# Performance work log

Measured on AMD Instinct MI355X. Metric: run time of the kernel, lower is better.

The kernel has to match this reference:

```python
import jax, jax.numpy as jnp
import numpy as np

N_NODES, N_EDGES, N_ANGLES, D = 20000, 200000, 600000, 128
BN_EPS = 1e-5
AGG_EPS = 1e-6


def _bn(x, gamma, beta):
    # training-mode BatchNorm1d over the node/edge batch dim
    mu = jnp.mean(x, axis=0)
    var = jnp.var(x, axis=0)
    return gamma * (x - mu) * jax.lax.rsqrt(var + BN_EPS) + beta


def _gcao(x, edge_index, y, W, b, bn):
    # Edge-gated graph conv (GCAO). W:[5,d,d] rows = src_gate, dst_gate,
    # edge_gate, src_update, dst_update. bn:[4,d] = gamma_n, beta_n, gamma_e, beta_e.
    src, dst = edge_index[0], edge_index[1]
    lin = lambda i, v: v @ W[i] + b[i]
    m = lin(0, x)[src] + lin(1, x)[dst] + lin(2, y)          # [E, d] edge messages
    sigma = jax.nn.sigmoid(m)                                 # edge gates
    bh = lin(3, x)[src] * sigma                               # gated src messages
    n = x.shape[0]
    num = jax.ops.segment_sum(bh, dst, num_segments=n)        # [N, d]
    den = jax.ops.segment_sum(sigma, dst, num_segments=n) + AGG_EPS
    x_new = x + jax.nn.silu(_bn(lin(4, x) + num / den, bn[0], bn[1]))
    y_new = y + jax.nn.silu(_bn(m, bn[2], bn[3]))
    return x_new, y_new


def setup_inputs() -> dict:
    key = jax.random.key(0)
    ks = jax.random.split(key, 8)
    s = 1.0 / np.sqrt(D)
    bn_init = jnp.stack([jnp.ones(D), jnp.zeros(D), jnp.ones(D), jnp.zeros(D)]).astype(jnp.float32)
    return {
        "atom_feats": jax.random.normal(ks[0], (N_NODES, D), jnp.float32),
        "bond_attr": jax.random.normal(ks[1], (N_EDGES, D), jnp.float32),
        "triplet_feats": jax.random.normal(ks[2], (N_ANGLES, D), jnp.float32),
        "edge_index": jax.random.randint(ks[3], (2, N_EDGES), 0, N_NODES),
        "angle_index": jax.random.randint(ks[4], (2, N_ANGLES), 0, N_EDGES),
        "W_ba": jax.random.normal(ks[5], (5, D, D), jnp.float32) * s,
        "b_ba": jnp.zeros((5, D), jnp.float32),
        "bn_ba": bn_init,
        "W_ab": jax.random.normal(ks[6], (5, D, D), jnp.float32) * s,
        "b_ab": jnp.zeros((5, D), jnp.float32),
        "bn_ab": bn_init,
    }


def reference(atom_feats, bond_attr, triplet_feats, edge_index, angle_index,
              W_ba, b_ba, bn_ba, W_ab, b_ab, bn_ab):
    # bondAndAngleUpdate: line graph (nodes=bonds, edges=angles)
    bond, trip = _gcao(bond_attr, angle_index, triplet_feats, W_ba, b_ba, bn_ba)
    # bondAndAtomUpdate: atom graph (nodes=atoms, edges=bonds)
    atom, bond_new = _gcao(atom_feats, edge_index, bond, W_ab, b_ab, bn_ab)
    return atom, bond_new, trip
```

## Files before the change

kernel.cpp:

```cpp
#include <hip/hip_runtime.h>
#include <hip/hip_bf16.h>


typedef float f32x4 __attribute__((ext_vector_type(4)));
typedef short s16x8 __attribute__((ext_vector_type(8)));
typedef unsigned short u16;

__device__ __forceinline__ u16 f2bf(float f){
  union { float f; unsigned u; } v; v.f = f;
  unsigned u = v.u;
  return (u16)((u + 0x7FFFu + ((u >> 16) & 1u)) >> 16);
}
__device__ __forceinline__ float bf2f(u16 h){
  union { unsigned u; float f; } v; v.u = ((unsigned)h) << 16; return v.f;
}
__device__ __forceinline__ float sigmoidf_(float x){ return 1.0f / (1.0f + __expf(-x)); }
__device__ __forceinline__ float siluf_(float x){ return x / (1.0f + __expf(-x)); }

__global__ __launch_bounds__(256) void pack_w_kernel(
    const float* __restrict__ Wba, const float* __restrict__ Wab, u16* __restrict__ wpack){
  int idx = blockIdx.x * 256 + threadIdx.x;
  int mat = idx >> 14;
  int r = idx & 16383;
  int j = r & 7, lane = (r >> 3) & 63, ks = (r >> 9) & 3, t = r >> 11;
  int k = ks * 32 + ((lane >> 4) << 3) + j;
  int n = t * 16 + (lane & 15);
  const float* W = (mat < 5) ? (Wba + (size_t)mat * 16384) : (Wab + (size_t)(mat - 5) * 16384);
  wpack[idx] = f2bf(W[k * 128 + n]);
}

__global__ __launch_bounds__(256) void xmm_kernel(
    const float* __restrict__ x, int nrows,
    const u16* __restrict__ wpackL, const float* __restrict__ bias,
    u16* __restrict__ L03, u16* __restrict__ L1, u16* __restrict__ L4){
  __shared__ u16 wlds[16384];
  const int tid = threadIdx.x;
  const int lane = tid & 63, wv = tid >> 6;
  const int g = lane >> 4;
  const long row = (long)blockIdx.x * 64 + wv * 16 + (lane & 15);
  const bool valid = row < nrows;
  const long rc = valid ? row : (long)(nrows - 1);

  s16x8 xf[4];
  {
    const float* xr = x + rc * 128 + g * 8;
    #pragma unroll
    for (int ks = 0; ks < 4; ++ks){
      float4 a = *(const float4*)(xr + ks * 32);
      float4 b = *(const float4*)(xr + ks * 32 + 4);
      s16x8 f;
      f[0]=(short)f2bf(a.x); f[1]=(short)f2bf(a.y); f[2]=(short)f2bf(a.z); f[3]=(short)f2bf(a.w);
      f[4]=(short)f2bf(b.x); f[5]=(short)f2bf(b.y); f[6]=(short)f2bf(b.z); f[7]=(short)f2bf(b.w);
      xf[ks] = f;
    }
  }
  const int mats[4] = {0, 1, 3, 4};
  #pragma unroll
  for (int mi = 0; mi < 4; ++mi){
    const int mat = mats[mi];
    __syncthreads();
    { const uint4* s = (const uint4*)(wpackL + (size_t)mat * 16384);
      uint4* d = (uint4*)wlds;
      #pragma unroll
      for (int i = 0; i < 8; ++i) d[i * 256 + tid] = s[i * 256 + tid];
    }
    __syncthreads();
    #pragma unroll
    for (int t = 0; t < 8; ++t){
      f32x4 acc = {0.f, 0.f, 0.f, 0.f};
      #pragma unroll
      for (int ks = 0; ks < 4; ++ks){
        s16x8 wf = *(const s16x8*)(wlds + (t * 4 + ks) * 512 + lane * 8);
        acc = __builtin_amdgcn_mfma_f32_16x16x32_bf16(wf, xf[ks], acc, 0, 0, 0);
      }
      const int c0 = t * 16 + g * 4;
      float4 bv = *(const float4*)(bias + mat * 128 + c0);
      if (valid){
        ushort4 o;
        o.x = f2bf(acc[0] + bv.x); o.y = f2bf(acc[1] + bv.y);
        o.z = f2bf(acc[2] + bv.z); o.w = f2bf(acc[3] + bv.w);
        u16* dp;
        if (mi == 0)      dp = L03 + row * 256 + c0;
        else if (mi == 1) dp = L1  + row * 128 + c0;
        else if (mi == 2) dp = L03 + row * 256 + 128 + c0;
        else              dp = L4  + row * 128 + c0;
        *(ushort4*)dp = o;
      }
    }
  }
}

__global__ __launch_bounds__(256) void edge_gemm_kernel(
    const float* __restrict__ y, const int* __restrict__ pos,
    const u16* __restrict__ wpack2, const float* __restrict__ bias2,
    u16* __restrict__ BH){
  __shared__ u16 wlds[16384];
  const int tid = threadIdx.x;
  { const uint4* s = (const uint4*)wpack2;
    uint4* d = (uint4*)wlds;
    #pragma unroll
    for (int i = 0; i < 8; ++i) d[i * 256 + tid] = s[i * 256 + tid];
  }
  const int lane = tid & 63, wv = tid >> 6;
  const int g = lane >> 4;
  const int e = blockIdx.x * 64 + wv * 16 + (lane & 15);
  const int p = pos[e];
  s16x8 yf[4];
  {
    const float* yr = y + (size_t)e * 128 + g * 8;
    #pragma unroll
    for (int ks = 0; ks < 4; ++ks){
      float4 a = *(const float4*)(yr + ks * 32);
      float4 b = *(const float4*)(yr + ks * 32 + 4);
      s16x8 f;
      f[0]=(short)f2bf(a.x); f[1]=(short)f2bf(a.y); f[2]=(short)f2bf(a.z); f[3]=(short)f2bf(a.w);
      f[4]=(short)f2bf(b.x); f[5]=(short)f2bf(b.y); f[6]=(short)f2bf(b.z); f[7]=(short)f2bf(b.w);
      yf[ks] = f;
    }
  }
  __syncthreads();
  u16* mrow = BH + (size_t)p * 128;
  #pragma unroll
  for (int t = 0; t < 8; ++t){
    f32x4 acc = {0.f, 0.f, 0.f, 0.f};
    #pragma unroll
    for (int ks = 0; ks < 4; ++ks){
      s16x8 wf = *(const s16x8*)(wlds + (t * 4 + ks) * 512 + lane * 8);
      acc = __builtin_amdgcn_mfma_f32_16x16x32_bf16(wf, yf[ks], acc, 0, 0, 0);
    }
    const int c0 = t * 16 + g * 4;
    float4 bv = *(const float4*)(bias2 + c0);
    ushort4 o;
    o.x = f2bf(acc[0] + bv.x); o.y = f2bf(acc[1] + bv.y);
    o.z = f2bf(acc[2] + bv.z); o.w = f2bf(acc[3] + bv.w);
    *(ushort4*)(mrow + c0) = o;
  }
}

__global__ __launch_bounds__(256) void combine_kernel(
    const int* __restrict__ src_csr, const int* __restrict__ dst_csr,
    const u16* __restrict__ L03, const u16* __restrict__ L1,
    u16* __restrict__ M, u16* __restrict__ BH){
  const int tid = threadIdx.x;
  const int wv = tid >> 6, half = (tid >> 5) & 1, ln = tid & 31;
  const int p = blockIdx.x * 8 + wv * 2 + half;
  const int c = ln * 4;
  const int src = src_csr[p];
  const int dst = dst_csr[p];
  ushort4 ma = *(const ushort4*)(BH + (size_t)p * 128 + c);
  ushort4 l0 = *(const ushort4*)(L03 + (size_t)src * 256 + c);
  ushort4 l3 = *(const ushort4*)(L03 + (size_t)src * 256 + 128 + c);
  ushort4 l1 = *(const ushort4*)(L1 + (size_t)dst * 128 + c);
  float m0 = bf2f(ma.x) + bf2f(l0.x) + bf2f(l1.x);
  float m1 = bf2f(ma.y) + bf2f(l0.y) + bf2f(l1.y);
  float m2 = bf2f(ma.z) + bf2f(l0.z) + bf2f(l1.z);
  float m3 = bf2f(ma.w) + bf2f(l0.w) + bf2f(l1.w);
  float g0 = sigmoidf_(m0), g1 = sigmoidf_(m1), g2 = sigmoidf_(m2), g3 = sigmoidf_(m3);
  ushort4 mo; mo.x = f2bf(m0); mo.y = f2bf(m1); mo.z = f2bf(m2); mo.w = f2bf(m3);
  ushort4 bo;
  bo.x = f2bf(bf2f(l3.x) * g0); bo.y = f2bf(bf2f(l3.y) * g1);
  bo.z = f2bf(bf2f(l3.z) * g2); bo.w = f2bf(bf2f(l3.w) * g3);
  *(ushort4*)(M + (size_t)p * 128 + c) = mo;
  *(ushort4*)(BH + (size_t)p * 128 + c) = bo;
}

__global__ __launch_bounds__(256) void hist_kernel(
    const int* __restrict__ dstIdx, int ne, int* __restrict__ count){
  int e = blockIdx.x * 256 + threadIdx.x;
  if (e < ne) atomicAdd(&count[dstIdx[e]], 1);
}

__global__ __launch_bounds__(256) void scan1_kernel(
    const int* __restrict__ count, int n, int* __restrict__ offset, int* __restrict__ bsum){
  __shared__ int sh[256];
  const int tid = threadIdx.x;
  const int i0 = blockIdx.x * 1024 + tid * 4;
  int c0 = (i0 + 0 < n) ? count[i0 + 0] : 0;
  int c1 = (i0 + 1 < n) ? count[i0 + 1] : 0;
  int c2 = (i0 + 2 < n) ? count[i0 + 2] : 0;
  int c3 = (i0 + 3 < n) ? count[i0 + 3] : 0;
  int tsum = c0 + c1 + c2 + c3;
  sh[tid] = tsum;
  __syncthreads();
  int val = tsum;
  for (int d = 1; d < 256; d <<= 1){
    int t = (tid >= d) ? sh[tid - d] : 0;
    __syncthreads();
    val += t;
    sh[tid] = val;
    __syncthreads();
  }
  int run = val - tsum;
  if (i0 + 0 < n) offset[i0 + 0] = run; run += c0;
  if (i0 + 1 < n) offset[i0 + 1] = run; run += c1;
  if (i0 + 2 < n) offset[i0 + 2] = run; run += c2;
  if (i0 + 3 < n) offset[i0 + 3] = run;
  if (tid == 255) bsum[blockIdx.x] = val;
}

__global__ __launch_bounds__(256) void scan2_kernel(int* __restrict__ bsum, int nb){
  __shared__ int sh[256];
  const int tid = threadIdx.x;
  int v = (tid < nb) ? bsum[tid] : 0;
  sh[tid] = v;
  __syncthreads();
  int val = v;
  for (int d = 1; d < 256; d <<= 1){
    int t = (tid >= d) ? sh[tid - d] : 0;
    __syncthreads();
    val += t;
    sh[tid] = val;
    __syncthreads();
  }
  if (tid < nb) bsum[tid] = val - v;
}

__global__ __launch_bounds__(256) void scan3_kernel(
    int* __restrict__ offset, int n, const int* __restrict__ bsum, int* __restrict__ cursor){
  int i = blockIdx.x * 256 + threadIdx.x;
  if (i < n){
    int v = offset[i] + bsum[i >> 10];
    offset[i] = v;
    cursor[i] = v;
  }
}

__global__ __launch_bounds__(256) void scatter_kernel(
    const int* __restrict__ dstIdx, const int* __restrict__ srcIdx, int ne,
    int* __restrict__ cursor, int* __restrict__ pos,
    int* __restrict__ src_csr, int* __restrict__ dst_csr){
  int e = blockIdx.x * 256 + threadIdx.x;
  if (e < ne){
    int d = dstIdx[e];
    int p = atomicAdd(&cursor[d], 1);
    pos[e] = p;
    src_csr[p] = srcIdx[e];
    dst_csr[p] = d;
  }
}

__global__ __launch_bounds__(256) void agg2_kernel(
    const int* __restrict__ offset, const int* __restrict__ count,
    const u16* __restrict__ M, const u16* __restrict__ BH,
    const u16* __restrict__ L4, int n, u16* __restrict__ hbuf){
  const int node = blockIdx.x * 4 + (threadIdx.x >> 6);
  if (node >= n) return;
  const int c2 = (threadIdx.x & 63) * 2;
  const int start = offset[node], deg = count[node];
  float n0 = 0, n1 = 0, d0 = 0, d1 = 0;
  int i = 0;
  for (; i + 2 <= deg; i += 2){
    const u16* mr = M + (size_t)(start + i) * 128;
    const u16* br = BH + (size_t)(start + i) * 128;
    ushort2 m0 = *(const ushort2*)(mr + c2);
    ushort2 m1 = *(const ushort2*)(mr + 128 + c2);
    ushort2 b0 = *(const ushort2*)(br + c2);
    ushort2 b1 = *(const ushort2*)(br + 128 + c2);
    float g00 = sigmoidf_(bf2f(m0.x)), g01 = sigmoidf_(bf2f(m0.y));
    float g10 = sigmoidf_(bf2f(m1.x)), g11 = sigmoidf_(bf2f(m1.y));
    d0 += g00 + g10; d1 += g01 + g11;
    n0 += bf2f(b0.x) + bf2f(b1.x); n1 += bf2f(b0.y) + bf2f(b1.y);
  }
  if (i < deg){
    const u16* mr = M + (size_t)(start + i) * 128;
    const u16* br = BH + (size_t)(start + i) * 128;
    ushort2 m0 = *(const ushort2*)(mr + c2);
    ushort2 b0 = *(const ushort2*)(br + c2);
    d0 += sigmoidf_(bf2f(m0.x)); d1 += sigmoidf_(bf2f(m0.y));
    n0 += bf2f(b0.x); n1 += bf2f(b0.y);
  }
  ushort2 l4 = *(const ushort2*)(L4 + (size_t)node * 128 + c2);
  float h0 = bf2f(l4.x) + n0 / (d0 + 1e-6f);
  float h1 = bf2f(l4.y) + n1 / (d1 + 1e-6f);
  ushort2 ho; ho.x = f2bf(h0); ho.y = f2bf(h1);
  *(ushort2*)(hbuf + (size_t)node * 128 + c2) = ho;
}

__global__ __launch_bounds__(256) void colstats_kernel(
    const u16* __restrict__ M, int rows, int rstride,
    float* __restrict__ sum, float* __restrict__ sumsq){
  const int tid = threadIdx.x;
  const int c2 = (tid & 63) * 2, rg = tid >> 6;
  float s0=0,ss0=0,s1=0,ss1=0;
  for (long r = blockIdx.x * 4 + rg; r < rows; r += (long)gridDim.x * 4){
    ushort2 v = *(const ushort2*)(M + r * rstride + c2);
    float a = bf2f(v.x), b = bf2f(v.y);
    s0 += a; ss0 += a*a; s1 += b; ss1 += b*b;
  }
  __shared__ float sh[1024];
  sh[tid] = s0; sh[256+tid] = ss0; sh[512+tid] = s1; sh[768+tid] = ss1;
  __syncthreads();
  if (rg == 0){
    int c = tid & 63;
    float S0=0,SS0=0,S1=0,SS1=0;
    #pragma unroll
    for (int q = 0; q < 4; ++q){ int t2 = q*64 + c; S0+=sh[t2]; SS0+=sh[256+t2]; S1+=sh[512+t2]; SS1+=sh[768+t2]; }
    atomicAdd(&sum[c2], S0);   atomicAdd(&sumsq[c2], SS0);
    atomicAdd(&sum[c2+1], S1); atomicAdd(&sumsq[c2+1], SS1);
  }
}

__global__ __launch_bounds__(256) void apply_bf16_kernel(
    const float* __restrict__ base, const u16* __restrict__ m, int n,
    const float* __restrict__ sum, const float* __restrict__ sumsq,
    const float* __restrict__ gamma, const float* __restrict__ beta,
    float* __restrict__ out){
  const int tid = threadIdx.x;
  const int c2 = (tid & 63) * 2, rg = tid >> 6;
  const float invn = 1.0f / (float)n;
  float m0 = sum[c2] * invn, m1 = sum[c2+1] * invn;
  float v0 = sumsq[c2] * invn - m0*m0, v1 = sumsq[c2+1] * invn - m1*m1;
  float sc0 = gamma[c2]   * rsqrtf(v0 + 1e-5f);
  float sc1 = gamma[c2+1] * rsqrtf(v1 + 1e-5f);
  float sh0 = beta[c2]   - m0 * sc0;
  float sh1 = beta[c2+1] - m1 * sc1;
  for (long r = blockIdx.x * 4 + rg; r < n; r += (long)gridDim.x * 4){
    const long bi = r * 128 + c2;
    ushort2 mv = *(const ushort2*)(m + bi);
    float2 xv = *(const float2*)(base + bi);
    float a = bf2f(mv.x) * sc0 + sh0, b = bf2f(mv.y) * sc1 + sh1;
    *(float2*)(out + bi) = make_float2(xv.x + siluf_(a), xv.y + siluf_(b));
  }
}

__global__ __launch_bounds__(256) void apply_perm_kernel(
    const float* __restrict__ base, const u16* __restrict__ M,
    const int* __restrict__ pos, int n,
    const float* __restrict__ sum, const float* __restrict__ sumsq,
    const float* __restrict__ gamma, const float* __restrict__ beta,
    float* __restrict__ out){
  const int tid = threadIdx.x;
  const int c2 = (tid & 63) * 2, rg = tid >> 6;
  const float invn = 1.0f / (float)n;
  float m0 = sum[c2] * invn, m1 = sum[c2+1] * invn;
  float v0 = sumsq[c2] * invn - m0*m0, v1 = sumsq[c2+1] * invn - m1*m1;
  float sc0 = gamma[c2]   * rsqrtf(v0 + 1e-5f);
  float sc1 = gamma[c2+1] * rsqrtf(v1 + 1e-5f);
  float sh0 = beta[c2]   - m0 * sc0;
  float sh1 = beta[c2+1] - m1 * sc1;
  for (long r = blockIdx.x * 4 + rg; r < n; r += (long)gridDim.x * 4){
    const int p = pos[r];
    ushort2 mv = *(const ushort2*)(M + (size_t)p * 128 + c2);
    float2 xv = *(const float2*)(base + r * 128 + c2);
    float a = bf2f(mv.x) * sc0 + sh0, b = bf2f(mv.y) * sc1 + sh1;
    *(float2*)(out + r * 128 + c2) = make_float2(xv.x + siluf_(a), xv.y + siluf_(b));
  }
}

extern "C" void kernel_launch(void* const* d_in, const int* in_sizes, int n_in,
                              void* d_out, int out_size, void* d_ws, size_t ws_size,
                              hipStream_t stream){
  const float* atom = (const float*)d_in[0];
  const float* bond = (const float*)d_in[1];
  const float* trip = (const float*)d_in[2];
  const int*   eidx = (const int*)d_in[3];
  const int*   aidx = (const int*)d_in[4];
  const float* Wba  = (const float*)d_in[5];
  const float* bba  = (const float*)d_in[6];
  const float* bnba = (const float*)d_in[7];
  const float* Wab  = (const float*)d_in[8];
  const float* bab  = (const float*)d_in[9];
  const float* bnab = (const float*)d_in[10];

  const int N = 20000, E = 200000, A = 600000;

  float* out_atom = (float*)d_out;
  float* out_bond = out_atom + (size_t)N * 128;
  float* out_trip = out_bond + (size_t)E * 128;

  char* ws = (char*)d_ws;
  u16* wpack = (u16*)ws;
  float* stats = (float*)(ws + 327680);
  float* sum_e = stats, *sumsq_e = stats + 128, *sum_n = stats + 256, *sumsq_n = stats + 384;
  int* bsum    = (int*)(ws + 329728);
  int* count   = (int*)(ws + 330752);
  int* offset  = (int*)(ws + 1130752);
  int* cursor  = (int*)(ws + 1930752);
  int* pos     = (int*)(ws + 2730752);
  int* src_csr = (int*)(ws + 5130752);
  int* dst_csr = (int*)(ws + 7530752);
  size_t off = 9930752;
  u16* L03 = (u16*)(ws + off); off += (size_t)E * 256 * 2;
  u16* L1  = (u16*)(ws + off); off += (size_t)E * 128 * 2;
  u16* L4  = (u16*)(ws + off); off += (size_t)E * 128 * 2;
  u16* M   = (u16*)(ws + off); off += (size_t)A * 128 * 2;
  u16* BH  = (u16*)(ws + off); off += (size_t)A * 128 * 2;
  u16* hbuf = L03;

  pack_w_kernel<<<640, 256, 0, stream>>>(Wba, Wab, wpack);

  {
    const int n = E, ne = A;
    const int* sIdx = aidx, *dIdx = aidx + A;
    hipMemsetAsync(stats, 0, 2048, stream);
    hipMemsetAsync(count, 0, (size_t)n * 4, stream);
    hist_kernel<<<(ne + 255) / 256, 256, 0, stream>>>(dIdx, ne, count);
    scan1_kernel<<<(n + 1023) / 1024, 256, 0, stream>>>(count, n, offset, bsum);
    scan2_kernel<<<1, 256, 0, stream>>>(bsum, (n + 1023) / 1024);
    scan3_kernel<<<(n + 255) / 256, 256, 0, stream>>>(offset, n, bsum, cursor);
    scatter_kernel<<<(ne + 255) / 256, 256, 0, stream>>>(dIdx, sIdx, ne, cursor, pos,
                                                         src_csr, dst_csr);
    xmm_kernel<<<n / 64, 256, 0, stream>>>(bond, n, wpack, bba, L03, L1, L4);
    edge_gemm_kernel<<<ne / 64, 256, 0, stream>>>(trip, pos, wpack + 2 * 16384,
                                                  bba + 256, BH);
    combine_kernel<<<ne / 8, 256, 0, stream>>>(src_csr, dst_csr, L03, L1, M, BH);
    colstats_kernel<<<1024, 256, 0, stream>>>(M, ne, 128, sum_e, sumsq_e);
    agg2_kernel<<<(n + 3) / 4, 256, 0, stream>>>(offset, count, M, BH, L4, n, hbuf);
    colstats_kernel<<<1024, 256, 0, stream>>>(hbuf, n, 128, sum_n, sumsq_n);
    apply_bf16_kernel<<<2048, 256, 0, stream>>>(bond, hbuf, n, sum_n, sumsq_n,
                                                bnba, bnba + 128, out_bond);
    apply_perm_kernel<<<2048, 256, 0, stream>>>(trip, M, pos, ne, sum_e, sumsq_e,
                                                bnba + 256, bnba + 384, out_trip);
  }

  {
    const int n = N, ne = E;
    const int* sIdx = eidx, *dIdx = eidx + E;
    hipMemsetAsync(stats, 0, 2048, stream);
    hipMemsetAsync(count, 0, (size_t)n * 4, stream);
    hist_kernel<<<(ne + 255) / 256, 256, 0, stream>>>(dIdx, ne, count);
    scan1_kernel<<<(n + 1023) / 1024, 256, 0, stream>>>(count, n, offset, bsum);
    scan2_kernel<<<1, 256, 0, stream>>>(bsum, (n + 1023) / 1024);
    scan3_kernel<<<(n + 255) / 256, 256, 0, stream>>>(offset, n, bsum, cursor);
    scatter_kernel<<<(ne + 255) / 256, 256, 0, stream>>>(dIdx, sIdx, ne, cursor, pos,
                                                         src_csr, dst_csr);
    xmm_kernel<<<(n + 63) / 64, 256, 0, stream>>>(atom, n, wpack + 5 * 16384, bab, L03, L1, L4);
    edge_gemm_kernel<<<ne / 64, 256, 0, stream>>>(out_bond, pos, wpack + 7 * 16384,
                                                  bab + 256, BH);
    combine_kernel<<<ne / 8, 256, 0, stream>>>(src_csr, dst_csr, L03, L1, M, BH);
    colstats_kernel<<<1024, 256, 0, stream>>>(M, ne, 128, sum_e, sumsq_e);
    agg2_kernel<<<(n + 3) / 4, 256, 0, stream>>>(offset, count, M, BH, L4, n, hbuf);
    colstats_kernel<<<1024, 256, 0, stream>>>(hbuf, n, 128, sum_n, sumsq_n);
    apply_bf16_kernel<<<2048, 256, 0, stream>>>(atom, hbuf, n, sum_n, sumsq_n,
                                                bnab, bnab + 128, out_atom);
    apply_perm_kernel<<<2048, 256, 0, stream>>>(out_bond, M, pos, ne, sum_e, sumsq_e,
                                                bnab + 256, bnab + 384, out_bond);
  }
}
```

Before: 1.227 ms.

## Fuse edge GEMM with gate combine, drop CSR src/dst arrays

Merges the edge-feature GEMM and the combine step into one kernel. The GEMM result is staged in LDS and combined with the gathered src/dst node projections in original edge order, and M and BH are written to their CSR positions. This removes a full bf16 round trip of the edge message through global memory and one launch, and lets scatter drop the src_csr/dst_csr writes. The two memsets are merged into one. In exchange, the extra LDS per block may lower occupancy.

```diff
diff --git a/kernel.cpp b/kernel.cpp
--- a/kernel.cpp
+++ b/kernel.cpp
@@ -90,11 +90,15 @@
   }
 }
 
-__global__ __launch_bounds__(256) void edge_gemm_kernel(
-    const float* __restrict__ y, const int* __restrict__ pos,
+__global__ __launch_bounds__(256) void edge_fused_kernel(
+    const float* __restrict__ y,
+    const int* __restrict__ srcIdx, const int* __restrict__ dstIdx,
+    const int* __restrict__ pos,
     const u16* __restrict__ wpack2, const float* __restrict__ bias2,
-    u16* __restrict__ BH){
+    const u16* __restrict__ L03, const u16* __restrict__ L1,
+    u16* __restrict__ M, u16* __restrict__ BH){
   __shared__ u16 wlds[16384];
+  __shared__ u16 mlds[64 * 132];
   const int tid = threadIdx.x;
   { const uint4* s = (const uint4*)wpack2;
     uint4* d = (uint4*)wlds;
@@ -103,8 +107,8 @@
   }
   const int lane = tid & 63, wv = tid >> 6;
   const int g = lane >> 4;
-  const int e = blockIdx.x * 64 + wv * 16 + (lane & 15);
-  const int p = pos[e];
+  const int erow = wv * 16 + (lane & 15);
+  const int e = blockIdx.x * 64 + erow;
   s16x8 yf[4];
   {
     const float* yr = y + (size_t)e * 128 + g * 8;
@@ -119,7 +123,6 @@
     }
   }
   __syncthreads();
-  u16* mrow = BH + (size_t)p * 128;
   #pragma unroll
   for (int t = 0; t < 8; ++t){
     f32x4 acc = {0.f, 0.f, 0.f, 0.f};
@@ -133,35 +136,34 @@
     ushort4 o;
     o.x = f2bf(acc[0] + bv.x); o.y = f2bf(acc[1] + bv.y);
     o.z = f2bf(acc[2] + bv.z); o.w = f2bf(acc[3] + bv.w);
-    *(ushort4*)(mrow + c0) = o;
-  }
-}
-
-__global__ __launch_bounds__(256) void combine_kernel(
-    const int* __restrict__ src_csr, const int* __restrict__ dst_csr,
-    const u16* __restrict__ L03, const u16* __restrict__ L1,
-    u16* __restrict__ M, u16* __restrict__ BH){
-  const int tid = threadIdx.x;
-  const int wv = tid >> 6, half = (tid >> 5) & 1, ln = tid & 31;
-  const int p = blockIdx.x * 8 + wv * 2 + half;
+    *(ushort4*)(mlds + erow * 132 + c0) = o;
+  }
+  __syncthreads();
+  const int hw = tid >> 5, ln = tid & 31;
   const int c = ln * 4;
-  const int src = src_csr[p];
-  const int dst = dst_csr[p];
-  ushort4 ma = *(const ushort4*)(BH + (size_t)p * 128 + c);
-  ushort4 l0 = *(const ushort4*)(L03 + (size_t)src * 256 + c);
-  ushort4 l3 = *(const ushort4*)(L03 + (size_t)src * 256 + 128 + c);
-  ushort4 l1 = *(const ushort4*)(L1 + (size_t)dst * 128 + c);
-  float m0 = bf2f(ma.x) + bf2f(l0.x) + bf2f(l1.x);
-  float m1 = bf2f(ma.y) + bf2f(l0.y) + bf2f(l1.y);
-  float m2 = bf2f(ma.z) + bf2f(l0.z) + bf2f(l1.z);
-  float m3 = bf2f(ma.w) + bf2f(l0.w) + bf2f(l1.w);
-  float g0 = sigmoidf_(m0), g1 = sigmoidf_(m1), g2 = sigmoidf_(m2), g3 = sigmoidf_(m3);
-  ushort4 mo; mo.x = f2bf(m0); mo.y = f2bf(m1); mo.z = f2bf(m2); mo.w = f2bf(m3);
-  ushort4 bo;
-  bo.x = f2bf(bf2f(l3.x) * g0); bo.y = f2bf(bf2f(l3.y) * g1);
-  bo.z = f2bf(bf2f(l3.z) * g2); bo.w = f2bf(bf2f(l3.w) * g3);
-  *(ushort4*)(M + (size_t)p * 128 + c) = mo;
-  *(ushort4*)(BH + (size_t)p * 128 + c) = bo;
+  #pragma unroll
+  for (int it = 0; it < 8; ++it){
+    const int es = it * 8 + hw;
+    const int ee = blockIdx.x * 64 + es;
+    const int p = pos[ee];
+    const int src = srcIdx[ee];
+    const int dst = dstIdx[ee];
+    ushort4 ma = *(const ushort4*)(mlds + es * 132 + c);
+    ushort4 l0 = *(const ushort4*)(L03 + (size_t)src * 256 + c);
+    ushort4 l3 = *(const ushort4*)(L03 + (size_t)src * 256 + 128 + c);
+    ushort4 l1 = *(const ushort4*)(L1 + (size_t)dst * 128 + c);
+    float m0 = bf2f(ma.x) + bf2f(l0.x) + bf2f(l1.x);
+    float m1 = bf2f(ma.y) + bf2f(l0.y) + bf2f(l1.y);
+    float m2 = bf2f(ma.z) + bf2f(l0.z) + bf2f(l1.z);
+    float m3 = bf2f(ma.w) + bf2f(l0.w) + bf2f(l1.w);
+    float g0 = sigmoidf_(m0), g1 = sigmoidf_(m1), g2 = sigmoidf_(m2), g3 = sigmoidf_(m3);
+    ushort4 mo; mo.x = f2bf(m0); mo.y = f2bf(m1); mo.z = f2bf(m2); mo.w = f2bf(m3);
+    ushort4 bo;
+    bo.x = f2bf(bf2f(l3.x) * g0); bo.y = f2bf(bf2f(l3.y) * g1);
+    bo.z = f2bf(bf2f(l3.z) * g2); bo.w = f2bf(bf2f(l3.w) * g3);
+    *(ushort4*)(M + (size_t)p * 128 + c) = mo;
+    *(ushort4*)(BH + (size_t)p * 128 + c) = bo;
+  }
 }
 
 __global__ __launch_bounds__(256) void hist_kernel(
@@ -226,16 +228,11 @@
 }
 
 __global__ __launch_bounds__(256) void scatter_kernel(
-    const int* __restrict__ dstIdx, const int* __restrict__ srcIdx, int ne,
-    int* __restrict__ cursor, int* __restrict__ pos,
-    int* __restrict__ src_csr, int* __restrict__ dst_csr){
+    const int* __restrict__ dstIdx, int ne,
+    int* __restrict__ cursor, int* __restrict__ pos){
   int e = blockIdx.x * 256 + threadIdx.x;
   if (e < ne){
-    int d = dstIdx[e];
-    int p = atomicAdd(&cursor[d], 1);
-    pos[e] = p;
-    src_csr[p] = srcIdx[e];
-    dst_csr[p] = d;
+    pos[e] = atomicAdd(&cursor[dstIdx[e]], 1);
   }
 }
 
@@ -377,9 +374,7 @@
   int* offset  = (int*)(ws + 1130752);
   int* cursor  = (int*)(ws + 1930752);
   int* pos     = (int*)(ws + 2730752);
-  int* src_csr = (int*)(ws + 5130752);
-  int* dst_csr = (int*)(ws + 7530752);
-  size_t off = 9930752;
+  size_t off = 5130752;
   u16* L03 = (u16*)(ws + off); off += (size_t)E * 256 * 2;
   u16* L1  = (u16*)(ws + off); off += (size_t)E * 128 * 2;
   u16* L4  = (u16*)(ws + off); off += (size_t)E * 128 * 2;
@@ -392,18 +387,16 @@
   {
     const int n = E, ne = A;
     const int* sIdx = aidx, *dIdx = aidx + A;
-    hipMemsetAsync(stats, 0, 2048, stream);
-    hipMemsetAsync(count, 0, (size_t)n * 4, stream);
+    hipMemsetAsync(stats, 0, 2048 + 1024 + (size_t)n * 4, stream);
     hist_kernel<<<(ne + 255) / 256, 256, 0, stream>>>(dIdx, ne, count);
     scan1_kernel<<<(n + 1023) / 1024, 256, 0, stream>>>(count, n, offset, bsum);
     scan2_kernel<<<1, 256, 0, stream>>>(bsum, (n + 1023) / 1024);
     scan3_kernel<<<(n + 255) / 256, 256, 0, stream>>>(offset, n, bsum, cursor);
-    scatter_kernel<<<(ne + 255) / 256, 256, 0, stream>>>(dIdx, sIdx, ne, cursor, pos,
-                                                         src_csr, dst_csr);
+    scatter_kernel<<<(ne + 255) / 256, 256, 0, stream>>>(dIdx, ne, cursor, pos);
     xmm_kernel<<<n / 64, 256, 0, stream>>>(bond, n, wpack, bba, L03, L1, L4);
-    edge_gemm_kernel<<<ne / 64, 256, 0, stream>>>(trip, pos, wpack + 2 * 16384,
-                                                  bba + 256, BH);
-    combine_kernel<<<ne / 8, 256, 0, stream>>>(src_csr, dst_csr, L03, L1, M, BH);
+    edge_fused_kernel<<<ne / 64, 256, 0, stream>>>(trip, sIdx, dIdx, pos,
+                                                   wpack + 2 * 16384, bba + 256,
+                                                   L03, L1, M, BH);
     colstats_kernel<<<1024, 256, 0, stream>>>(M, ne, 128, sum_e, sumsq_e);
     agg2_kernel<<<(n + 3) / 4, 256, 0, stream>>>(offset, count, M, BH, L4, n, hbuf);
     colstats_kernel<<<1024, 256, 0, stream>>>(hbuf, n, 128, sum_n, sumsq_n);
@@ -416,18 +409,16 @@
   {
     const int n = N, ne = E;
     const int* sIdx = eidx, *dIdx = eidx + E;
-    hipMemsetAsync(stats, 0, 2048, stream);
-    hipMemsetAsync(count, 0, (size_t)n * 4, stream);
+    hipMemsetAsync(stats, 0, 2048 + 1024 + (size_t)n * 4, stream);
     hist_kernel<<<(ne + 255) / 256, 256, 0, stream>>>(dIdx, ne, count);
     scan1_kernel<<<(n + 1023) / 1024, 256, 0, stream>>>(count, n, offset, bsum);
     scan2_kernel<<<1, 256, 0, stream>>>(bsum, (n + 1023) / 1024);
     scan3_kernel<<<(n + 255) / 256, 256, 0, stream>>>(offset, n, bsum, cursor);
-    scatter_kernel<<<(ne + 255) / 256, 256, 0, stream>>>(dIdx, sIdx, ne, cursor, pos,
-                                                         src_csr, dst_csr);
+    scatter_kernel<<<(ne + 255) / 256, 256, 0, stream>>>(dIdx, ne, cursor, pos);
     xmm_kernel<<<(n + 63) / 64, 256, 0, stream>>>(atom, n, wpack + 5 * 16384, bab, L03, L1, L4);
-    edge_gemm_kernel<<<ne / 64, 256, 0, stream>>>(out_bond, pos, wpack + 7 * 16384,
-                                                  bab + 256, BH);
-    combine_kernel<<<ne / 8, 256, 0, stream>>>(src_csr, dst_csr, L03, L1, M, BH);
+    edge_fused_kernel<<<ne / 64, 256, 0, stream>>>(out_bond, sIdx, dIdx, pos,
+                                                   wpack + 7 * 16384, bab + 256,
+                                                   L03, L1, M, BH);
     colstats_kernel<<<1024, 256, 0, stream>>>(M, ne, 128, sum_e, sumsq_e);
     agg2_kernel<<<(n + 3) / 4, 256, 0, stream>>>(offset, count, M, BH, L4, n, hbuf);
     colstats_kernel<<<1024, 256, 0, stream>>>(hbuf, n, 128, sum_n, sumsq_n);
```

After: 1.132 ms. 7.8% less time.
